# Kernel tuning notes

Measured on AMD Instinct MI355X. Metric: run time of the kernel, lower is better.

Reference implementation:

```python
import jax, jax.numpy as jnp
import numpy as np


def rotary_pos_emb(x):
    # x: [b, h, l, k]; interleaved rotary embedding (pairs are (0,1),(2,3),...)
    dim = x.shape[-1]
    seq = x.shape[-2]
    ts = jnp.arange(0, dim, 2, dtype=jnp.float32)
    inv_freqs = 10000.0 ** (-ts / dim)                      # [dim/2]
    grid = jnp.arange(seq, dtype=jnp.float32)[:, None] * inv_freqs[None, :]  # [l, dim/2]
    sin_embs = jnp.repeat(jnp.sin(grid), 2, axis=-1)[None]  # [1, l, dim] (interleaved repeat)
    cos_embs = jnp.repeat(jnp.cos(grid), 2, axis=-1)[None]
    x1, x2 = x[..., ::2], x[..., 1::2]
    xs = jnp.stack([-x2, x1], axis=-1).reshape(x.shape)     # interleave (-x2, x1)
    return x * cos_embs + xs * sin_embs


def setup_inputs() -> dict:
    key = jax.random.key(0)
    ks = jax.random.split(key, 5)
    b, l, d = 2, 2048, 1024
    scale = 1.0 / np.sqrt(d)
    return {
        "x": jax.random.normal(ks[0], (b, l, d), dtype=jnp.float32),
        "Wq": jax.random.normal(ks[1], (d, d), dtype=jnp.float32) * scale,
        "Wk": jax.random.normal(ks[2], (d, d), dtype=jnp.float32) * scale,
        "Wv": jax.random.normal(ks[3], (d, d), dtype=jnp.float32) * scale,
        "Wo": jax.random.normal(ks[4], (d, d), dtype=jnp.float32) * scale,
        "is_training": 0,
    }


def reference(x, Wq, Wk, Wv, Wo, is_training):
    n_heads = 16
    b, l, d = x.shape
    k_size = d // n_heads
    # NOTE: module scales q by 1/sqrt(model_size), not 1/sqrt(key_size)
    q = (x @ Wq) / jnp.sqrt(jnp.float32(d))
    q = q.reshape(b, l, n_heads, k_size).transpose(0, 2, 1, 3)  # b h l k
    k = (x @ Wk).reshape(b, l, n_heads, k_size).transpose(0, 2, 1, 3)
    v = (x @ Wv).reshape(b, l, n_heads, k_size).transpose(0, 2, 1, 3)
    q = rotary_pos_emb(q)
    k = rotary_pos_emb(k)
    logits = jnp.einsum('bhik,bhjk->bhij', q, k)  # no mask, no dropout (eval)
    a = jax.nn.softmax(logits, axis=-1)
    y = jnp.einsum('bhij,bhjv->bhiv', a, v)
    y = y.transpose(0, 2, 1, 3).reshape(b, l, d)  # b l (h v)
    return y @ Wo
```

## Files before the change

### kernel.cpp

```cpp
#include <hip/hip_runtime.h>
#include <stdint.h>

typedef unsigned short u16;
typedef unsigned int u32;
using short8 = __attribute__((ext_vector_type(8))) short;
using f32x4  = __attribute__((ext_vector_type(4))) float;
using f32x16 = __attribute__((ext_vector_type(16))) float;

typedef __attribute__((address_space(1))) unsigned int gu32;
typedef __attribute__((address_space(3))) unsigned int lu32;

__device__ __forceinline__ void gl2lds16(const u16* g, u16* lds_wave_base) {
    __builtin_amdgcn_global_load_lds(
        (gu32*)(uintptr_t)(const void*)g,
        (lu32*)(uint32_t)(uintptr_t)(void*)lds_wave_base,
        16, 0, 0);
}

__device__ inline float bf2f(u16 u) {
    union { unsigned int i; float f; } v;
    v.i = ((unsigned int)u) << 16;
    return v.f;
}
__device__ inline u16 f2bf(float f) {
    union { float f; unsigned int i; } v;
    v.f = f;
    unsigned int x = v.i;
    return (u16)((x + 0x7fffu + ((x >> 16) & 1u)) >> 16);
}
__device__ inline u32 f2bf_trunc_u32(float f) {
    union { float f; unsigned int i; } v;
    v.f = f;
    return v.i >> 16;
}

__global__ __launch_bounds__(256) void prep(
    const float* __restrict__ x, u16* __restrict__ xb,
    const float* __restrict__ w0, const float* __restrict__ w1,
    const float* __restrict__ w2, const float* __restrict__ w3,
    u16* __restrict__ t0, u16* __restrict__ t1,
    u16* __restrict__ t2, u16* __restrict__ t3,
    float2* __restrict__ tab)
{
    int tx = threadIdx.x, ty = threadIdx.y;
    int tid = ty * 32 + tx;
    int z = blockIdx.z;
    if (z == 4) {
        int bidx = blockIdx.y * 32 + blockIdx.x;
        if (bidx < 256) {
            int idx = bidx * 256 + tid;
            int pos = idx >> 5, pi = idx & 31;
            const float l2_10000_over_32 = 0.41524101186f;
            float ang = (float)pos *
                __builtin_amdgcn_exp2f(-(float)pi * l2_10000_over_32);
            float sn, cs;
            __sincosf(ang, &sn, &cs);
            tab[idx] = make_float2(cs, sn);
        }
        return;
    }
    if (z >= 5) {
        int i = (((z - 5) * 1024 + blockIdx.y * 32 + blockIdx.x) * 256 + tid) * 4;
        float4 v = *(const float4*)(x + i);
        ushort4 o;
        o.x = f2bf(v.x); o.y = f2bf(v.y); o.z = f2bf(v.z); o.w = f2bf(v.w);
        *(ushort4*)(xb + i) = o;
        return;
    }
    __shared__ u16 tile[32][33];
    const float* src; u16* dst;
    switch (z) {
        case 0:  src = w0; dst = t0; break;
        case 1:  src = w1; dst = t1; break;
        case 2:  src = w2; dst = t2; break;
        default: src = w3; dst = t3; break;
    }
    int c0 = blockIdx.x * 32, r0 = blockIdx.y * 32;
    #pragma unroll
    for (int i = 0; i < 4; i++)
        tile[ty + i * 8][tx] = f2bf(src[(size_t)(r0 + ty + i * 8) * 1024 + c0 + tx]);
    __syncthreads();
    #pragma unroll
    for (int i = 0; i < 4; i++)
        dst[(size_t)(c0 + ty + i * 8) * 1024 + r0 + tx] = tile[tx][ty + i * 8];
}

__global__ __launch_bounds__(256) void gemm_qkv(
    const u16* __restrict__ A, const u16* __restrict__ Bt,
    const float2* __restrict__ ropetab,
    u16* __restrict__ Qb, u16* __restrict__ Kb, u16* __restrict__ VT)
{
    __shared__ __align__(16) char smem[128 * 136 * 2];
    u16* As = (u16*)smem;
    u16* Bs = (u16*)(smem + 16384);

    const int tid  = threadIdx.x;
    const int lane = tid & 63;
    const int wid  = tid >> 6;
    const int quad = lane >> 4;
    const int l15  = lane & 15;
    const int wm   = wid >> 1, wn = wid & 1;

    const int m0 = blockIdx.y * 128;
    const int n0 = blockIdx.x * 128;
    const int mat = n0 >> 10;
    const int ln0 = n0 & 1023;

    f32x4 acc[4][4] = {};

    for (int k0 = 0; k0 < 1024; k0 += 64) {
        #pragma unroll
        for (int it = 0; it < 4; it++) {
            int c   = it * 256 + tid;
            int row = c >> 3;
            int col = ((c & 7) ^ (row & 7)) * 8;
            u16* lbA = &As[(size_t)(it * 256 + wid * 64) * 8];
            u16* lbB = &Bs[(size_t)(it * 256 + wid * 64) * 8];
            gl2lds16(&A [(size_t)(m0 + row) * 1024 + k0 + col], lbA);
            gl2lds16(&Bt[(size_t)(n0 + row) * 1024 + k0 + col], lbB);
        }
        __syncthreads();

        #pragma unroll
        for (int s = 0; s < 2; s++) {
            short8 a[4], b[4];
            #pragma unroll
            for (int i = 0; i < 4; i++) {
                int ra = wm * 64 + i * 16 + l15;
                int rb = wn * 64 + i * 16 + l15;
                a[i] = *(const short8*)(&As[ra * 64 + (((s * 4 + quad) ^ (ra & 7)) * 8)]);
                b[i] = *(const short8*)(&Bs[rb * 64 + (((s * 4 + quad) ^ (rb & 7)) * 8)]);
            }
            #pragma unroll
            for (int i = 0; i < 4; i++)
                #pragma unroll
                for (int j = 0; j < 4; j++)
                    acc[i][j] = __builtin_amdgcn_mfma_f32_16x16x32_bf16(a[i], b[j], acc[i][j], 0, 0, 0);
        }
        __syncthreads();
    }

    if (mat < 2) {
        u16* C = (mat == 0) ? Qb : Kb;
        const float scale = (mat == 0) ? (0.03125f * 1.44269504f) : 1.0f;
        const int odd = l15 & 1;
        #pragma unroll
        for (int i = 0; i < 4; i++)
            #pragma unroll
            for (int j = 0; j < 4; j++)
                #pragma unroll
                for (int r = 0; r < 4; r++) {
                    int lrow = wm * 64 + i * 16 + quad * 4 + r;
                    int col  = ln0 + wn * 64 + j * 16 + l15;
                    int pos  = (m0 + lrow) & 2047;
                    float v  = acc[i][j][r] * scale;
                    float vp = __shfl_xor(v, 1);
                    float2 sc = ropetab[pos * 32 + ((col & 63) >> 1)];
                    float outv = odd ? (v * sc.x + vp * sc.y)
                                     : (v * sc.x - vp * sc.y);
                    C[(size_t)(m0 + lrow) * 1024 + col] = f2bf(outv);
                }
    } else {
        u16* T = (u16*)smem;
        __syncthreads();
        #pragma unroll
        for (int i = 0; i < 4; i++)
            #pragma unroll
            for (int j = 0; j < 4; j++)
                #pragma unroll
                for (int r = 0; r < 4; r++) {
                    int lrow = wm * 64 + i * 16 + quad * 4 + r;
                    int lcol = wn * 64 + j * 16 + l15;
                    T[lcol * 136 + lrow] = f2bf(acc[i][j][r]);
                }
        __syncthreads();
        int bb2 = m0 >> 11, pos0 = m0 & 2047;
        #pragma unroll
        for (int itc = 0; itc < 8; itc++) {
            int c  = itc * 256 + tid;
            int ch = c >> 4;
            int px = (c & 15) * 8;
            int head = (ln0 + ch) >> 6;
            size_t dst = ((size_t)(bb2 * 16 + head) * 64 + (ch & 63)) * 2048
                         + pos0 + px;
            *(uint4*)(&VT[dst]) = *(const uint4*)(&T[ch * 136 + px]);
        }
    }
}

__global__ __launch_bounds__(256) void gemm_out(
    const u16* __restrict__ A, const u16* __restrict__ Bt, float* __restrict__ C)
{
    __shared__ __align__(16) u16 As[128 * 64];
    __shared__ __align__(16) u16 Bs[128 * 64];

    const int tid  = threadIdx.x;
    const int lane = tid & 63;
    const int wid  = tid >> 6;
    const int quad = lane >> 4;
    const int l15  = lane & 15;
    const int wm   = wid >> 1, wn = wid & 1;

    const int m0 = blockIdx.y * 128;
    const int n0 = blockIdx.x * 128;

    f32x4 acc[4][4] = {};

    for (int k0 = 0; k0 < 1024; k0 += 64) {
        #pragma unroll
        for (int it = 0; it < 4; it++) {
            int c   = it * 256 + tid;
            int row = c >> 3;
            int col = ((c & 7) ^ (row & 7)) * 8;
            u16* lbA = &As[(size_t)(it * 256 + wid * 64) * 8];
            u16* lbB = &Bs[(size_t)(it * 256 + wid * 64) * 8];
            gl2lds16(&A [(size_t)(m0 + row) * 1024 + k0 + col], lbA);
            gl2lds16(&Bt[(size_t)(n0 + row) * 1024 + k0 + col], lbB);
        }
        __syncthreads();

        #pragma unroll
        for (int s = 0; s < 2; s++) {
            short8 a[4], b[4];
            #pragma unroll
            for (int i = 0; i < 4; i++) {
                int ra = wm * 64 + i * 16 + l15;
                int rb = wn * 64 + i * 16 + l15;
                a[i] = *(const short8*)(&As[ra * 64 + (((s * 4 + quad) ^ (ra & 7)) * 8)]);
                b[i] = *(const short8*)(&Bs[rb * 64 + (((s * 4 + quad) ^ (rb & 7)) * 8)]);
            }
            #pragma unroll
            for (int i = 0; i < 4; i++)
                #pragma unroll
                for (int j = 0; j < 4; j++)
                    acc[i][j] = __builtin_amdgcn_mfma_f32_16x16x32_bf16(a[i], b[j], acc[i][j], 0, 0, 0);
        }
        __syncthreads();
    }

    #pragma unroll
    for (int i = 0; i < 4; i++)
        #pragma unroll
        for (int j = 0; j < 4; j++)
            #pragma unroll
            for (int r = 0; r < 4; r++) {
                int row = m0 + wm * 64 + i * 16 + quad * 4 + r;
                int col = n0 + wn * 64 + j * 16 + l15;
                C[(size_t)row * 1024 + col] = acc[i][j][r];
            }
}

__global__ __launch_bounds__(256) void attn(
    const u16* __restrict__ Q, const u16* __restrict__ Kb,
    const u16* __restrict__ VT, u16* __restrict__ Y)
{
    __shared__ __align__(16) u16 Ks [128 * 64];
    __shared__ __align__(16) u16 VTs[64 * 128];
    __shared__ __align__(16) u16 Ps [4][32 * 72];

    const int tid  = threadIdx.x;
    const int lane = tid & 63, wid = tid >> 6;
    const int l31  = lane & 31, hi = lane >> 5;

    const int bh = blockIdx.x;
    const int qt = blockIdx.y;
    const int bb = bh >> 4, h = bh & 15;

    const size_t base = ((size_t)bb * 2048) * 1024 + (size_t)h * 64;

    short8 qf[4];
    {
        const u16* qp = Q + base
                      + ((size_t)qt * 128 + wid * 32 + l31) * 1024 + hi * 8;
        #pragma unroll
        for (int s = 0; s < 4; s++)
            qf[s] = *(const short8*)(qp + s * 16);
    }

    f32x16 o0 = {}, o1 = {};
    float lsum = 0.0f;

    for (int j0 = 0; j0 < 2048; j0 += 128) {
        __syncthreads();
        #pragma unroll
        for (int it = 0; it < 4; it++) {
            int c = it * 256 + tid;
            int rk = c >> 3, ck = ((c & 7)  ^ (rk & 7))  * 8;
            int rv = c >> 4, cv = ((c & 15) ^ (rv & 15)) * 8;
            u16* lbK = &Ks [(size_t)(it * 256 + wid * 64) * 8];
            u16* lbV = &VTs[(size_t)(it * 256 + wid * 64) * 8];
            gl2lds16(&Kb[base + (size_t)(j0 + rk) * 1024 + ck], lbK);
            gl2lds16(&VT[((size_t)bh * 64 + rv) * 2048 + j0 + cv], lbV);
        }
        __syncthreads();

        f32x16 st[4];
        #pragma unroll
        for (int t = 0; t < 4; t++) {
            int key = t * 32 + l31;
            f32x16 z = {};
            #pragma unroll
            for (int s = 0; s < 4; s++) {
                int chunk = ((2 * s + hi) ^ (key & 7)) * 8;
                short8 kf = *(const short8*)(&Ks[key * 64 + chunk]);
                z = __builtin_amdgcn_mfma_f32_32x32x16_bf16(kf, qf[s], z, 0, 0, 0);
            }
            st[t] = z;
        }

        u16* ps = Ps[wid];
        #pragma unroll
        for (int hh = 0; hh < 2; hh++) {
            #pragma unroll
            for (int tt = 0; tt < 2; tt++) {
                int t = hh * 2 + tt;
                #pragma unroll
                for (int g = 0; g < 4; g++) {
                    float p0 = __builtin_amdgcn_exp2f(st[t][4 * g + 0]);
                    float p1 = __builtin_amdgcn_exp2f(st[t][4 * g + 1]);
                    float p2 = __builtin_amdgcn_exp2f(st[t][4 * g + 2]);
                    float p3 = __builtin_amdgcn_exp2f(st[t][4 * g + 3]);
                    lsum += (p0 + p1) + (p2 + p3);
                    uint2 w;
                    w.x = f2bf_trunc_u32(p0) | (f2bf_trunc_u32(p1) << 16);
                    w.y = f2bf_trunc_u32(p2) | (f2bf_trunc_u32(p3) << 16);
                    int lk = tt * 32 + g * 8 + hi * 4;
                    *(uint2*)(&ps[l31 * 72 + lk]) = w;
                }
            }
            asm volatile("s_waitcnt lgkmcnt(0)" ::: "memory");

            #pragma unroll
            for (int s = 0; s < 4; s++) {
                int koff = s * 16 + hi * 8;
                short8 pf = *(const short8*)(&ps[l31 * 72 + koff]);
                int kch = hh * 8 + 2 * s + hi;
                short8 v0 = *(const short8*)(&VTs[l31 * 128 + ((kch ^ (l31 & 15)) * 8)]);
                short8 v1 = *(const short8*)(&VTs[(32 + l31) * 128 + ((kch ^ ((32 + l31) & 15)) * 8)]);
                o0 = __builtin_amdgcn_mfma_f32_32x32x16_bf16(pf, v0, o0, 0, 0, 0);
                o1 = __builtin_amdgcn_mfma_f32_32x32x16_bf16(pf, v1, o1, 0, 0, 0);
            }
            asm volatile("" ::: "memory");
        }
    }

    lsum += __shfl_xor(lsum, 32);
    float linv = 1.0f / lsum;

    size_t qrow0 = (size_t)qt * 128 + wid * 32;
    #pragma unroll
    for (int half = 0; half < 2; half++) {
        f32x16 o = half ? o1 : o0;
        #pragma unroll
        for (int reg = 0; reg < 16; reg++) {
            int qrow = (reg & 3) + 8 * (reg >> 2) + 4 * hi;
            float nv = o[reg] * __shfl(linv, qrow);
            Y[base + (qrow0 + qrow) * 1024 + half * 32 + l31] = f2bf(nv);
        }
    }
}

extern "C" void kernel_launch(void* const* d_in, const int* in_sizes, int n_in,
                              void* d_out, int out_size, void* d_ws, size_t ws_size,
                              hipStream_t stream)
{
    const float* x  = (const float*)d_in[0];
    const float* Wq = (const float*)d_in[1];
    const float* Wk = (const float*)d_in[2];
    const float* Wv = (const float*)d_in[3];
    const float* Wo = (const float*)d_in[4];
    float* out = (float*)d_out;

    char* ws = (char*)d_ws;
    u16*    xb    = (u16*)   (ws + (0ull  << 20));
    u16*    WqkvT = (u16*)   (ws + (8ull  << 20));
    u16*    WoT   = (u16*)   (ws + (14ull << 20));
    u16*    Qb    = (u16*)   (ws + (16ull << 20));
    u16*    Kb    = (u16*)   (ws + (24ull << 20));
    u16*    VTb   = (u16*)   (ws + (32ull << 20));
    u16*    Yb    = (u16*)   (ws + (40ull << 20));
    float2* tab   = (float2*)(ws + (48ull << 20));

    prep<<<dim3(32, 32, 9), dim3(32, 8), 0, stream>>>(
        x, xb, Wq, Wk, Wv, Wo,
        WqkvT, WqkvT + (1024ull * 1024), WqkvT + (2048ull * 1024), WoT, tab);
    gemm_qkv<<<dim3(24, 32), 256, 0, stream>>>(xb, WqkvT, tab, Qb, Kb, VTb);
    attn<<<dim3(32, 16), 256, 0, stream>>>(Qb, Kb, VTb, Yb);
    gemm_out<<<dim3(8, 32), 256, 0, stream>>>(Yb, WoT, out);
}
```

Before: 202.0 us.

## Split attention key tile across wave pairs and reduce partial outputs in LDS

Each block now handles 64 query rows instead of 128. The pair of waves sharing a 32-row query group each processes half of every 128-key tile. At the end they exchange partial O accumulators and row sums through LDS, then each writes one 32-column half of the output. This doubles the grid to 1024 blocks for better occupancy and load balance across CUs. The cost is that the K/V tile loads are amortized over half as many queries, which doubles global/LDS K/V traffic, and it adds an extra reduction phase.

```diff
diff --git a/kernel.cpp b/kernel.cpp
--- a/kernel.cpp
+++ b/kernel.cpp
@@ -256,11 +256,13 @@
 {
     __shared__ __align__(16) u16 Ks [128 * 64];
     __shared__ __align__(16) u16 VTs[64 * 128];
-    __shared__ __align__(16) u16 Ps [4][32 * 72];
+    __shared__ __align__(16) u16 Ps [4][32 * 68];
 
     const int tid  = threadIdx.x;
     const int lane = tid & 63, wid = tid >> 6;
     const int l31  = lane & 31, hi = lane >> 5;
+    const int rg   = wid >> 1;
+    const int wk   = wid & 1;
 
     const int bh = blockIdx.x;
     const int qt = blockIdx.y;
@@ -271,7 +273,7 @@
     short8 qf[4];
     {
         const u16* qp = Q + base
-                      + ((size_t)qt * 128 + wid * 32 + l31) * 1024 + hi * 8;
+                      + ((size_t)qt * 64 + rg * 32 + l31) * 1024 + hi * 8;
         #pragma unroll
         for (int s = 0; s < 4; s++)
             qf[s] = *(const short8*)(qp + s * 16);
@@ -294,10 +296,10 @@
         }
         __syncthreads();
 
-        f32x16 st[4];
-        #pragma unroll
-        for (int t = 0; t < 4; t++) {
-            int key = t * 32 + l31;
+        f32x16 st[2];
+        #pragma unroll
+        for (int t = 0; t < 2; t++) {
+            int key = wk * 64 + t * 32 + l31;
             f32x16 z = {};
             #pragma unroll
             for (int s = 0; s < 4; s++) {
@@ -310,53 +312,66 @@
 
         u16* ps = Ps[wid];
         #pragma unroll
-        for (int hh = 0; hh < 2; hh++) {
-            #pragma unroll
-            for (int tt = 0; tt < 2; tt++) {
-                int t = hh * 2 + tt;
-                #pragma unroll
-                for (int g = 0; g < 4; g++) {
-                    float p0 = __builtin_amdgcn_exp2f(st[t][4 * g + 0]);
-                    float p1 = __builtin_amdgcn_exp2f(st[t][4 * g + 1]);
-                    float p2 = __builtin_amdgcn_exp2f(st[t][4 * g + 2]);
-                    float p3 = __builtin_amdgcn_exp2f(st[t][4 * g + 3]);
-                    lsum += (p0 + p1) + (p2 + p3);
-                    uint2 w;
-                    w.x = f2bf_trunc_u32(p0) | (f2bf_trunc_u32(p1) << 16);
-                    w.y = f2bf_trunc_u32(p2) | (f2bf_trunc_u32(p3) << 16);
-                    int lk = tt * 32 + g * 8 + hi * 4;
-                    *(uint2*)(&ps[l31 * 72 + lk]) = w;
-                }
+        for (int tt = 0; tt < 2; tt++) {
+            #pragma unroll
+            for (int g = 0; g < 4; g++) {
+                float p0 = __builtin_amdgcn_exp2f(st[tt][4 * g + 0]);
+                float p1 = __builtin_amdgcn_exp2f(st[tt][4 * g + 1]);
+                float p2 = __builtin_amdgcn_exp2f(st[tt][4 * g + 2]);
+                float p3 = __builtin_amdgcn_exp2f(st[tt][4 * g + 3]);
+                lsum += (p0 + p1) + (p2 + p3);
+                uint2 w;
+                w.x = f2bf_trunc_u32(p0) | (f2bf_trunc_u32(p1) << 16);
+                w.y = f2bf_trunc_u32(p2) | (f2bf_trunc_u32(p3) << 16);
+                int lk = tt * 32 + g * 8 + hi * 4;
+                *(uint2*)(&ps[l31 * 68 + lk]) = w;
             }
-            asm volatile("s_waitcnt lgkmcnt(0)" ::: "memory");
-
-            #pragma unroll
-            for (int s = 0; s < 4; s++) {
-                int koff = s * 16 + hi * 8;
-                short8 pf = *(const short8*)(&ps[l31 * 72 + koff]);
-                int kch = hh * 8 + 2 * s + hi;
-                short8 v0 = *(const short8*)(&VTs[l31 * 128 + ((kch ^ (l31 & 15)) * 8)]);
-                short8 v1 = *(const short8*)(&VTs[(32 + l31) * 128 + ((kch ^ ((32 + l31) & 15)) * 8)]);
-                o0 = __builtin_amdgcn_mfma_f32_32x32x16_bf16(pf, v0, o0, 0, 0, 0);
-                o1 = __builtin_amdgcn_mfma_f32_32x32x16_bf16(pf, v1, o1, 0, 0, 0);
-            }
-            asm volatile("" ::: "memory");
-        }
+        }
+        asm volatile("s_waitcnt lgkmcnt(0)" ::: "memory");
+
+        #pragma unroll
+        for (int s = 0; s < 4; s++) {
+            int koff = s * 16 + hi * 8;
+            short8 pf = *(const short8*)(&ps[l31 * 68 + koff]);
+            int kch = wk * 8 + 2 * s + hi;
+            short8 v0 = *(const short8*)(&VTs[l31 * 128 + ((kch ^ (l31 & 15)) * 8)]);
+            short8 v1 = *(const short8*)(&VTs[(32 + l31) * 128 + ((kch ^ ((32 + l31) & 15)) * 8)]);
+            o0 = __builtin_amdgcn_mfma_f32_32x32x16_bf16(pf, v0, o0, 0, 0, 0);
+            o1 = __builtin_amdgcn_mfma_f32_32x32x16_bf16(pf, v1, o1, 0, 0, 0);
+        }
+        asm volatile("" ::: "memory");
     }
 
     lsum += __shfl_xor(lsum, 32);
-    float linv = 1.0f / lsum;
-
-    size_t qrow0 = (size_t)qt * 128 + wid * 32;
+
+    __syncthreads();
+    float* xo = (float*)Ks;
+    float* lb = (float*)VTs;
+    {
+        f32x16 give = wk ? o0 : o1;
+        float* wb = xo + wid * 1024;
+        #pragma unroll
+        for (int r = 0; r < 16; r++)
+            wb[r * 64 + lane] = give[r];
+        if (hi == 0) lb[wid * 32 + l31] = lsum;
+    }
+    __syncthreads();
+    const int pw = wid ^ 1;
+    f32x16 keep = wk ? o1 : o0;
+    {
+        const float* rb = xo + pw * 1024;
+        #pragma unroll
+        for (int r = 0; r < 16; r++)
+            keep[r] += rb[r * 64 + lane];
+    }
+    float linv = 1.0f / (lsum + lb[pw * 32 + l31]);
+
+    const size_t qrow0 = (size_t)qt * 64 + rg * 32;
     #pragma unroll
-    for (int half = 0; half < 2; half++) {
-        f32x16 o = half ? o1 : o0;
-        #pragma unroll
-        for (int reg = 0; reg < 16; reg++) {
-            int qrow = (reg & 3) + 8 * (reg >> 2) + 4 * hi;
-            float nv = o[reg] * __shfl(linv, qrow);
-            Y[base + (qrow0 + qrow) * 1024 + half * 32 + l31] = f2bf(nv);
-        }
+    for (int reg = 0; reg < 16; reg++) {
+        int qrow = (reg & 3) + 8 * (reg >> 2) + 4 * hi;
+        float nv = keep[reg] * __shfl(linv, qrow);
+        Y[base + (qrow0 + qrow) * 1024 + wk * 32 + l31] = f2bf(nv);
     }
 }
 
@@ -385,6 +400,6 @@
         x, xb, Wq, Wk, Wv, Wo,
         WqkvT, WqkvT + (1024ull * 1024), WqkvT + (2048ull * 1024), WoT, tab);
     gemm_qkv<<<dim3(24, 32), 256, 0, stream>>>(xb, WqkvT, tab, Qb, Kb, VTb);
-    attn<<<dim3(32, 16), 256, 0, stream>>>(Qb, Kb, VTb, Yb);
+    attn<<<dim3(32, 32), 256, 0, stream>>>(Qb, Kb, VTb, Yb);
     gemm_out<<<dim3(8, 32), 256, 0, stream>>>(Yb, WoT, out);
 }
```

Measured after the change: 226.7 us. 12.3% more time.

## Double-buffer K/V tiles and widen attention blocks to eight waves

Applied to the files above, without the earlier changes.

The attention kernel now runs 512 threads per block covering 256 query rows, so each K/V tile staged in LDS serves twice as many waves. K and V^T are double-buffered, and the next tile is prefetched with global_load_lds while the current one is computed, with explicit vmcnt waits and barriers replacing the old load-then-sync pattern. The P scratch row stride changes from 72 to 68. This halves the grid to 256 blocks and roughly doubles LDS use per block, which may lower occupancy or leave CUs idle, and the new stride may change LDS bank conflicts.

```diff
diff --git a/kernel.cpp b/kernel.cpp
--- a/kernel.cpp
+++ b/kernel.cpp
@@ -250,13 +250,13 @@
             }
 }
 
-__global__ __launch_bounds__(256) void attn(
+__global__ __launch_bounds__(512) void attn(
     const u16* __restrict__ Q, const u16* __restrict__ Kb,
     const u16* __restrict__ VT, u16* __restrict__ Y)
 {
-    __shared__ __align__(16) u16 Ks [128 * 64];
-    __shared__ __align__(16) u16 VTs[64 * 128];
-    __shared__ __align__(16) u16 Ps [4][32 * 72];
+    __shared__ __align__(16) u16 Ks [2][128 * 64];
+    __shared__ __align__(16) u16 VTs[2][64 * 128];
+    __shared__ __align__(16) u16 Ps [8][32 * 68];
 
     const int tid  = threadIdx.x;
     const int lane = tid & 63, wid = tid >> 6;
@@ -271,28 +271,41 @@
     short8 qf[4];
     {
         const u16* qp = Q + base
-                      + ((size_t)qt * 128 + wid * 32 + l31) * 1024 + hi * 8;
+                      + ((size_t)qt * 256 + wid * 32 + l31) * 1024 + hi * 8;
         #pragma unroll
         for (int s = 0; s < 4; s++)
             qf[s] = *(const short8*)(qp + s * 16);
     }
+    asm volatile("s_waitcnt vmcnt(0)" ::: "memory");
+
+    auto stage = [&](int jt, int b) {
+        #pragma unroll
+        for (int it = 0; it < 2; it++) {
+            int c  = it * 512 + tid;
+            int rk = c >> 3, ck = ((c & 7)  ^ (rk & 7))  * 8;
+            int rv = c >> 4, cv = ((c & 15) ^ (rv & 15)) * 8;
+            u16* lbK = &Ks [b][(size_t)(it * 512 + wid * 64) * 8];
+            u16* lbV = &VTs[b][(size_t)(it * 512 + wid * 64) * 8];
+            gl2lds16(&Kb[base + (size_t)(jt * 128 + rk) * 1024 + ck], lbK);
+            gl2lds16(&VT[((size_t)bh * 64 + rv) * 2048 + jt * 128 + cv], lbV);
+        }
+    };
 
     f32x16 o0 = {}, o1 = {};
     float lsum = 0.0f;
 
-    for (int j0 = 0; j0 < 2048; j0 += 128) {
-        __syncthreads();
-        #pragma unroll
-        for (int it = 0; it < 4; it++) {
-            int c = it * 256 + tid;
-            int rk = c >> 3, ck = ((c & 7)  ^ (rk & 7))  * 8;
-            int rv = c >> 4, cv = ((c & 15) ^ (rv & 15)) * 8;
-            u16* lbK = &Ks [(size_t)(it * 256 + wid * 64) * 8];
-            u16* lbV = &VTs[(size_t)(it * 256 + wid * 64) * 8];
-            gl2lds16(&Kb[base + (size_t)(j0 + rk) * 1024 + ck], lbK);
-            gl2lds16(&VT[((size_t)bh * 64 + rv) * 2048 + j0 + cv], lbV);
-        }
-        __syncthreads();
+    stage(0, 0);
+
+    for (int j = 0; j < 16; ++j) {
+        const int cb = j & 1;
+        if (j < 15) {
+            stage(j + 1, cb ^ 1);
+            asm volatile("s_waitcnt vmcnt(4)" ::: "memory");
+        } else {
+            asm volatile("s_waitcnt vmcnt(0)" ::: "memory");
+        }
+        __builtin_amdgcn_s_barrier();
+        asm volatile("" ::: "memory");
 
         f32x16 st[4];
         #pragma unroll
@@ -302,7 +315,7 @@
             #pragma unroll
             for (int s = 0; s < 4; s++) {
                 int chunk = ((2 * s + hi) ^ (key & 7)) * 8;
-                short8 kf = *(const short8*)(&Ks[key * 64 + chunk]);
+                short8 kf = *(const short8*)(&Ks[cb][key * 64 + chunk]);
                 z = __builtin_amdgcn_mfma_f32_32x32x16_bf16(kf, qf[s], z, 0, 0, 0);
             }
             st[t] = z;
@@ -325,7 +338,7 @@
                     w.x = f2bf_trunc_u32(p0) | (f2bf_trunc_u32(p1) << 16);
                     w.y = f2bf_trunc_u32(p2) | (f2bf_trunc_u32(p3) << 16);
                     int lk = tt * 32 + g * 8 + hi * 4;
-                    *(uint2*)(&ps[l31 * 72 + lk]) = w;
+                    *(uint2*)(&ps[l31 * 68 + lk]) = w;
                 }
             }
             asm volatile("s_waitcnt lgkmcnt(0)" ::: "memory");
@@ -333,21 +346,25 @@
             #pragma unroll
             for (int s = 0; s < 4; s++) {
                 int koff = s * 16 + hi * 8;
-                short8 pf = *(const short8*)(&ps[l31 * 72 + koff]);
+                short8 pf = *(const short8*)(&ps[l31 * 68 + koff]);
                 int kch = hh * 8 + 2 * s + hi;
-                short8 v0 = *(const short8*)(&VTs[l31 * 128 + ((kch ^ (l31 & 15)) * 8)]);
-                short8 v1 = *(const short8*)(&VTs[(32 + l31) * 128 + ((kch ^ ((32 + l31) & 15)) * 8)]);
+                short8 v0 = *(const short8*)(&VTs[cb][l31 * 128 + ((kch ^ (l31 & 15)) * 8)]);
+                short8 v1 = *(const short8*)(&VTs[cb][(32 + l31) * 128 + ((kch ^ ((32 + l31) & 15)) * 8)]);
                 o0 = __builtin_amdgcn_mfma_f32_32x32x16_bf16(pf, v0, o0, 0, 0, 0);
                 o1 = __builtin_amdgcn_mfma_f32_32x32x16_bf16(pf, v1, o1, 0, 0, 0);
             }
             asm volatile("" ::: "memory");
         }
+
+        asm volatile("s_waitcnt lgkmcnt(0)" ::: "memory");
+        __builtin_amdgcn_s_barrier();
+        asm volatile("" ::: "memory");
     }
 
     lsum += __shfl_xor(lsum, 32);
     float linv = 1.0f / lsum;
 
-    size_t qrow0 = (size_t)qt * 128 + wid * 32;
+    const size_t qrow0 = (size_t)qt * 256 + wid * 32;
     #pragma unroll
     for (int half = 0; half < 2; half++) {
         f32x16 o = half ? o1 : o0;
@@ -385,6 +402,6 @@
         x, xb, Wq, Wk, Wv, Wo,
         WqkvT, WqkvT + (1024ull * 1024), WqkvT + (2048ull * 1024), WoT, tab);
     gemm_qkv<<<dim3(24, 32), 256, 0, stream>>>(xb, WqkvT, tab, Qb, Kb, VTb);
-    attn<<<dim3(32, 16), 256, 0, stream>>>(Qb, Kb, VTb, Yb);
+    attn<<<dim3(32, 8), 512, 0, stream>>>(Qb, Kb, VTb, Yb);
     gemm_out<<<dim3(8, 32), 256, 0, stream>>>(Yb, WoT, out);
 }
```

After: 212.4 us. +5.2%, slower.
